# Performance work log

Hardware: AMD Instinct MI355X
Metric: run time of the kernel (lower is better)

## Reference

```python
import math
import jax, jax.numpy as jnp
import numpy as np

B, S, E, H = 2, 2048, 1024, 16
DK = E // H

def setup_inputs() -> dict:
    key = jax.random.key(0)
    ks = jax.random.split(key, 12)
    sc = 1.0 / math.sqrt(E)
    return {
        "x": jax.random.normal(ks[0], (B, S, E), jnp.float32),
        "kv": jax.random.normal(ks[1], (B, S, E), jnp.float32),
        "mask": jax.random.randint(ks[2], (B, S), 0, 2, jnp.int32),
        "attn_bias": jax.random.normal(ks[3], (B, S, S), jnp.float32),
        "WQ_w": jax.random.normal(ks[4], (E, E), jnp.float32) * sc,
        "WQ_b": jnp.zeros((E,), jnp.float32),
        "WK_w": jax.random.normal(ks[5], (E, E), jnp.float32) * sc,
        "WK_b": jnp.zeros((E,), jnp.float32),
        "WV_w": jax.random.normal(ks[6], (E, E), jnp.float32) * sc,
        "WV_b": jnp.zeros((E,), jnp.float32),
        "WO_w": jax.random.normal(ks[7], (E, E), jnp.float32) * sc,
        "WO_b": jnp.zeros((E,), jnp.float32),
    }

def reference(x, kv, mask, attn_bias, WQ_w, WQ_b, WK_w, WK_b, WV_w, WV_b, WO_w, WO_b):
    b, sq, _ = x.shape
    sk = kv.shape[1]
    # projections, split heads: [B,S,E] -> [B,H,S,DK]
    Q = (x @ WQ_w.T + WQ_b).reshape(b, sq, H, DK).transpose(0, 2, 1, 3)
    K = (kv @ WK_w.T + WK_b).reshape(b, sk, H, DK).transpose(0, 2, 1, 3)
    V = (kv @ WV_w.T + WV_b).reshape(b, sk, H, DK).transpose(0, 2, 1, 3)
    # scores [B,H,Sq,Sk]
    T = jnp.einsum('bhqd,bhkd->bhqk', Q, K) / math.sqrt(DK)
    T = T + attn_bias[:, None, :, :]  # 3D bias broadcast over heads
    m2 = jnp.einsum('bi,bj->bij', mask.astype(T.dtype), mask.astype(T.dtype))
    T = jnp.where(m2[:, None, :, :] == 0, jnp.asarray(-1e9, T.dtype), T)
    A = jax.nn.softmax(T, axis=-1)
    out = jnp.einsum('bhqk,bhkd->bhqd', A, V)  # [B,H,Sq,DK]
    out = out.transpose(0, 2, 1, 3).reshape(b, sq, E)
    return out @ WO_w.T + WO_b
```

## Files before the change

kernel.cpp:

```cpp
#include <hip/hip_runtime.h>

#define DEV static __device__ __forceinline__

typedef __attribute__((ext_vector_type(8))) __bf16 bf16x8;
typedef __attribute__((ext_vector_type(4))) float f32x4;

constexpr int CB = 2;
constexpr int CS = 2048;
constexpr int CE = 1024;
constexpr int CH = 16;
constexpr int CD = 64;
constexpr float LOG2E = 1.44269504f;

DEV unsigned short f2bf(float x) {
  unsigned int u = __float_as_uint(x);
  u += 0x7fffu + ((u >> 16) & 1u);
  return (unsigned short)(u >> 16);
}

DEV f32x4 mfma32(bf16x8 a, bf16x8 b, f32x4 c) {
  return __builtin_amdgcn_mfma_f32_16x16x32_bf16(a, b, c, 0, 0, 0);
}

DEV unsigned int cvtpk(float lo, float hi) {
  unsigned int r;
  asm("v_cvt_pk_bf16_f32 %0, %1, %2" : "=v"(r) : "v"(lo), "v"(hi));
  return r;
}

DEV float exp2r(float x) {
#if __has_builtin(__builtin_amdgcn_exp2f)
  return __builtin_amdgcn_exp2f(x);
#else
  float r; asm("v_exp_f32 %0, %1" : "=v"(r) : "v"(x)); return r;
#endif
}

DEV f32x4 unpk(unsigned int a, unsigned int b) {
  f32x4 r;
  r[0] = __uint_as_float(a << 16);
  r[1] = __uint_as_float(a & 0xffff0000u);
  r[2] = __uint_as_float(b << 16);
  r[3] = __uint_as_float(b & 0xffff0000u);
  return r;
}

DEV void stage16(const void* g, void* l) {
  __builtin_amdgcn_global_load_lds(
      (const __attribute__((address_space(1))) unsigned int*)g,
      (__attribute__((address_space(3))) unsigned int*)l, 16, 0, 0);
}

DEV void cvt_body(long i, const float* __restrict__ x, const float* __restrict__ kv,
                  const float* __restrict__ w0, const float* __restrict__ w1,
                  const float* __restrict__ w2, const float* __restrict__ w3,
                  unsigned short* __restrict__ out) {
  const long NE = (long)CB * CS * CE;
  const long WE = (long)CE * CE;
  const float* src;
  long off = i;
  if (i < NE) {
    src = x;
  } else if (i < 2 * NE) {
    src = kv; off = i - NE;
  } else {
    long j = i - 2 * NE;
    int wi = (int)(j >> 20);
    src = wi == 0 ? w0 : wi == 1 ? w1 : wi == 2 ? w2 : w3;
    off = j & (WE - 1);
  }
  float4 a = *reinterpret_cast<const float4*>(src + off);
  float4 b = *reinterpret_cast<const float4*>(src + off + 4);
  uint4 v;
  v.x = (unsigned int)f2bf(a.x) | ((unsigned int)f2bf(a.y) << 16);
  v.y = (unsigned int)f2bf(a.z) | ((unsigned int)f2bf(a.w) << 16);
  v.z = (unsigned int)f2bf(b.x) | ((unsigned int)f2bf(b.y) << 16);
  v.w = (unsigned int)f2bf(b.z) | ((unsigned int)f2bf(b.w) << 16);
  *reinterpret_cast<uint4*>(out + i) = v;
}

DEV void mbias_body(long idx, const float* __restrict__ bias, const int* __restrict__ mask,
                    unsigned short* __restrict__ mb16) {
  const int b = (int)(idx >> 22);
  const int q = (int)((idx >> 11) & (CS - 1));
  const int k0 = (int)(idx & (CS - 1));
  const bool mq = mask[b * CS + q] != 0;
  const int4 mk0 = *reinterpret_cast<const int4*>(mask + b * CS + k0);
  const int4 mk1 = *reinterpret_cast<const int4*>(mask + b * CS + k0 + 4);
  const float4 b0 = *reinterpret_cast<const float4*>(bias + idx);
  const float4 b1 = *reinterpret_cast<const float4*>(bias + idx + 4);
  const float NEG = -1e9f * LOG2E;
  float v[8];
  if (mq) {
    v[0] = (mk0.x != 0) ? b0.x * LOG2E : NEG;
    v[1] = (mk0.y != 0) ? b0.y * LOG2E : NEG;
    v[2] = (mk0.z != 0) ? b0.z * LOG2E : NEG;
    v[3] = (mk0.w != 0) ? b0.w * LOG2E : NEG;
    v[4] = (mk1.x != 0) ? b1.x * LOG2E : NEG;
    v[5] = (mk1.y != 0) ? b1.y * LOG2E : NEG;
    v[6] = (mk1.z != 0) ? b1.z * LOG2E : NEG;
    v[7] = (mk1.w != 0) ? b1.w * LOG2E : NEG;
  } else {
#pragma unroll
    for (int j = 0; j < 8; j++) v[j] = 0.f;
  }
  uint4 o;
  o.x = cvtpk(v[0], v[1]); o.y = cvtpk(v[2], v[3]);
  o.z = cvtpk(v[4], v[5]); o.w = cvtpk(v[6], v[7]);
  *reinterpret_cast<uint4*>(mb16 + idx) = o;
}

__global__ __launch_bounds__(256) void prep_all(const float* __restrict__ x,
                                                const float* __restrict__ kv,
                                                const float* __restrict__ w0,
                                                const float* __restrict__ w1,
                                                const float* __restrict__ w2,
                                                const float* __restrict__ w3,
                                                unsigned short* __restrict__ outcvt,
                                                const float* __restrict__ bias,
                                                const int* __restrict__ mask,
                                                unsigned short* __restrict__ mb16) {
  const long CVTB = (2 * (long)CB * CS * CE + 4 * (long)CE * CE) / 2048;
  if (blockIdx.x < CVTB) {
    cvt_body(((long)blockIdx.x * 256 + threadIdx.x) * 8, x, kv, w0, w1, w2, w3, outcvt);
  } else {
    mbias_body(((long)(blockIdx.x - CVTB) * 256 + threadIdx.x) * 8, bias, mask, mb16);
  }
}

__global__ __launch_bounds__(256) void cvt_all(const float* __restrict__ x,
                                               const float* __restrict__ kv,
                                               const float* __restrict__ w0,
                                               const float* __restrict__ w1,
                                               const float* __restrict__ w2,
                                               const float* __restrict__ w3,
                                               unsigned short* __restrict__ out) {
  cvt_body(((long)blockIdx.x * 256 + threadIdx.x) * 8, x, kv, w0, w1, w2, w3, out);
}
__global__ __launch_bounds__(256) void mk_mbias(const float* __restrict__ bias,
                                                const int* __restrict__ mask,
                                                unsigned short* __restrict__ mb16) {
  mbias_body(((long)blockIdx.x * 256 + threadIdx.x) * 8, bias, mask, mb16);
}

__global__ __launch_bounds__(512) void gemm_qkv(const unsigned short* __restrict__ xb,
                                                const unsigned short* __restrict__ kvb,
                                                const unsigned short* __restrict__ Wall,
                                                const float* __restrict__ bq,
                                                const float* __restrict__ bk,
                                                const float* __restrict__ bv,
                                                unsigned short* __restrict__ Qb) {
  __shared__ __align__(16) unsigned char ldsA[32768];
  __shared__ __align__(16) unsigned char ldsB[32768];
  const long NE = (long)CB * CS * CE;
  const long WE = (long)CE * CE;
  const int which = blockIdx.y >> 2;
  const int n0 = (blockIdx.y & 3) * 256;
  const int m0 = blockIdx.x * 256;
  const unsigned char* Ab = (const unsigned char*)(which == 0 ? xb : kvb);
  const unsigned char* Bb = (const unsigned char*)(Wall + (long)which * WE);
  const float* bias = which == 0 ? bq : which == 1 ? bk : bv;

  const int tid = threadIdx.x;
  const int lane = tid & 63, w = tid >> 6;
  const int wr = w >> 2, wc = w & 3;
  const int g = lane >> 4, rr = lane & 15;

  const int srow = tid >> 2;
  const int scsw = ((tid & 3) * 16) ^ (((tid >> 5) & 1) << 5);
  const unsigned char* apR0 = Ab + ((long)(m0 + srow) * CE) * 2 + scsw;
  const unsigned char* apR1 = Ab + ((long)(m0 + 128 + srow) * CE) * 2 + scsw;
  const unsigned char* bpR0 = Bb + ((long)(n0 + srow) * CE) * 2 + scsw;
  const unsigned char* bpR1 = Bb + ((long)(n0 + 128 + srow) * CE) * 2 + scsw;

  const int cswz = (g * 16) ^ (((rr >> 3) & 1) << 5);
  const unsigned char* rbA = ldsA + wr * 8192 + rr * 64 + cswz;
  const unsigned char* rbB = ldsB + wc * 4096 + rr * 64 + cswz;

  f32x4 acc[8][4] = {};

  auto stA = [&](int buf) {
    stage16(apR0, ldsA + buf * 16384 + w * 1024);
    stage16(apR1, ldsA + buf * 16384 + 8192 + w * 1024);
    apR0 += 64; apR1 += 64;
  };
  auto stB = [&](int buf) {
    stage16(bpR0, ldsB + buf * 16384 + w * 1024);
    stage16(bpR1, ldsB + buf * 16384 + 8192 + w * 1024);
    bpR0 += 64; bpR1 += 64;
  };

  stB(0);
  stA(0);
  stB(1);
  asm volatile("s_waitcnt vmcnt(3)" ::: "memory");
  __builtin_amdgcn_s_barrier();

  auto group = [&](int buf) {
    bf16x8 ar[4], br[4];
#pragma unroll
    for (int ii = 0; ii < 4; ii++)
      ar[ii] = *reinterpret_cast<const bf16x8*>(rbA + buf * 16384 + ii * 1024);
#pragma unroll
    for (int j = 0; j < 4; j++)
      br[j] = *reinterpret_cast<const bf16x8*>(rbB + buf * 16384 + j * 1024);
    stA(buf ^ 1);
    __builtin_amdgcn_s_barrier();
    asm volatile("s_waitcnt lgkmcnt(0)" ::: "memory");
    __builtin_amdgcn_sched_barrier(0);
    __builtin_amdgcn_s_setprio(1);
#pragma unroll
    for (int ii = 0; ii < 4; ii++)
#pragma unroll
      for (int j = 0; j < 4; j++)
        acc[ii][j] = mfma32(ar[ii], br[j], acc[ii][j]);
    __builtin_amdgcn_s_setprio(0);
    asm volatile("s_waitcnt vmcnt(4)" ::: "memory");
    __builtin_amdgcn_s_barrier();
#pragma unroll
    for (int ii = 0; ii < 4; ii++)
      ar[ii] = *reinterpret_cast<const bf16x8*>(rbA + buf * 16384 + 4096 + ii * 1024);
    stB(buf);
    __builtin_amdgcn_s_barrier();
    asm volatile("s_waitcnt lgkmcnt(0)" ::: "memory");
    __builtin_amdgcn_sched_barrier(0);
    __builtin_amdgcn_s_setprio(1);
#pragma unroll
    for (int ii = 0; ii < 4; ii++)
#pragma unroll
      for (int j = 0; j < 4; j++)
        acc[4 + ii][j] = mfma32(ar[ii], br[j], acc[4 + ii][j]);
    __builtin_amdgcn_s_setprio(0);
    asm volatile("s_waitcnt vmcnt(3)" ::: "memory");
    __builtin_amdgcn_s_barrier();
  };

#pragma unroll 1
  for (int it = 0; it < 16; ++it) {
    group(0);
    group(1);
  }
  asm volatile("s_waitcnt vmcnt(0)" ::: "memory");

  const float scale = which == 0 ? 0.125f * LOG2E : 1.0f;
#pragma unroll
  for (int i = 0; i < 8; i++) {
#pragma unroll
    for (int j = 0; j < 4; j++) {
      const int colg = n0 + wc * 64 + j * 16 + rr;
      const float bvv = bias[colg];
      if (which == 2) {
        const int rowbase = m0 + wr * 128 + i * 16 + g * 4;
        const int bb = rowbase >> 11, s = rowbase & 2047;
        const int hh = colg >> 6, d = colg & 63;
        uint2 val;
        val.x = (unsigned int)f2bf(acc[i][j][0] + bvv) | ((unsigned int)f2bf(acc[i][j][1] + bvv) << 16);
        val.y = (unsigned int)f2bf(acc[i][j][2] + bvv) | ((unsigned int)f2bf(acc[i][j][3] + bvv) << 16);
        *reinterpret_cast<uint2*>(Qb + 2 * NE + ((long)((bb * CH + hh) * CD + d)) * CS + s) = val;
      } else {
        unsigned short* outp = Qb + (long)which * NE;
#pragma unroll
        for (int r = 0; r < 4; r++) {
          const int row = m0 + wr * 128 + i * 16 + g * 4 + r;
          outp[(long)row * CE + colg] = f2bf((acc[i][j][r] + bvv) * scale);
        }
      }
    }
  }
}

__global__ __launch_bounds__(256) void gemm_wo(const unsigned short* __restrict__ A,
                                               const unsigned short* __restrict__ W,
                                               const float* __restrict__ bias,
                                               float* __restrict__ out) {
  __shared__ __align__(16) unsigned short As[128 * 64];
  __shared__ __align__(16) unsigned short Bs[64 * 64];
  const int tid = threadIdx.x;
  const int lane = tid & 63, wave = tid >> 6;
  const int wm = (wave >> 1) * 64, wn = (wave & 1) * 32;
  const int g = lane >> 4, rr = lane & 15;
  const int m0 = blockIdx.x * 128, n0 = blockIdx.y * 64;
  const int K = CE;
  f32x4 acc[4][2] = {};

  for (int k0 = 0; k0 < K; k0 += 64) {
#pragma unroll
    for (int t = 0; t < 4; t++) {
      const int u = t * 256 + tid;
      const int row = u >> 3, ce = (u & 7) * 8;
      stage16(A + (long)(m0 + row) * K + k0 + ce, (char*)As + (t * 256 + (tid & 192)) * 16);
    }
#pragma unroll
    for (int t = 0; t < 2; t++) {
      const int u = t * 256 + tid;
      const int row = u >> 3, ce = (u & 7) * 8;
      stage16(W + (long)(n0 + row) * K + k0 + ce, (char*)Bs + (t * 256 + (tid & 192)) * 16);
    }
    __syncthreads();
#pragma unroll
    for (int kk = 0; kk < 2; kk++) {
      bf16x8 af[4], bfr[2];
#pragma unroll
      for (int i = 0; i < 4; i++)
        af[i] = *reinterpret_cast<const bf16x8*>(&As[(wm + i * 16 + rr) * 64 + kk * 32 + g * 8]);
#pragma unroll
      for (int j = 0; j < 2; j++)
        bfr[j] = *reinterpret_cast<const bf16x8*>(&Bs[(wn + j * 16 + rr) * 64 + kk * 32 + g * 8]);
#pragma unroll
      for (int i = 0; i < 4; i++)
#pragma unroll
        for (int j = 0; j < 2; j++)
          acc[i][j] = mfma32(af[i], bfr[j], acc[i][j]);
    }
    __syncthreads();
  }

#pragma unroll
  for (int i = 0; i < 4; i++)
#pragma unroll
    for (int j = 0; j < 2; j++) {
      const int colg = n0 + wn + j * 16 + rr;
      const float bvv = bias[colg];
#pragma unroll
      for (int r = 0; r < 4; r++) {
        const int row = m0 + wm + i * 16 + g * 4 + r;
        out[(long)row * CE + colg] = acc[i][j][r] + bvv;
      }
    }
}

__global__ __launch_bounds__(256, 2) void attn_kernel(const unsigned short* __restrict__ Qb,
                                                      const unsigned short* __restrict__ Kb,
                                                      const unsigned short* __restrict__ Vtw,
                                                      const unsigned short* __restrict__ mb16,
                                                      const int* __restrict__ mask,
                                                      unsigned short* __restrict__ AO) {
  __shared__ __align__(16) unsigned char lds[65536];
  const int h = blockIdx.x, qt = blockIdx.y, b = blockIdx.z;
  const int tid = threadIdx.x;
  const int lane = tid & 63, w = tid >> 6;
  const int g = lane >> 4, c = lane & 15;
  const int qbase = qt * 128 + w * 32;

  bf16x8 qf[2][2];
#pragma unroll
  for (int qb = 0; qb < 2; qb++) {
    const unsigned short* Qrow = Qb + ((long)b * CS + qbase + qb * 16 + c) * CE + h * CD;
    qf[qb][0] = *reinterpret_cast<const bf16x8*>(Qrow + g * 8);
    qf[qb][1] = *reinterpret_cast<const bf16x8*>(Qrow + 32 + g * 8);
    if (mask[b * CS + qbase + qb * 16 + c] == 0) {
      qf[qb][0] = bf16x8{}; qf[qb][1] = bf16x8{};
    }
  }

  const unsigned char *kg[4], *vg[4];
  {
    const unsigned char* Ksrc = (const unsigned char*)(Kb + (long)b * CS * CE + h * CD);
    const unsigned char* Vsrc = (const unsigned char*)(Vtw + (long)(b * CH + h) * CD * CS);
    const int rr8 = lane >> 3;
    const int csw = ((lane & 7) << 4) ^ (rr8 << 4);
#pragma unroll
    for (int t = 0; t < 4; t++) {
      const int krow = t * 32 + w * 8 + rr8;
      const int key = (krow & 96) + ((krow >> 2) & 3) * 8 + ((krow >> 4) & 1) * 4 + (krow & 3);
      kg[t] = Ksrc + (long)key * (CE * 2) + csw;
      const int vrow = (t & 1) * 32 + w * 8 + rr8;
      vg[t] = Vsrc + (long)vrow * (CS * 2) + (t >> 1) * 128 + csw;
    }
  }
  const int sw = (c & 7) << 4;
  const unsigned char* rb0 = lds + c * 128 + ((g * 16) ^ sw);
  const unsigned char* rb1 = lds + c * 128 + ((64 + g * 16) ^ sw);

  const unsigned short* mbp0 = mb16 + ((long)b * CS + qbase + c) * CS + g * 8;
  const unsigned short* mbp1 = mb16 + ((long)b * CS + qbase + 16 + c) * CS + g * 8;

  f32x4 o[2][4] = {};
  f32x4 lsum4[2] = {};
  uint4 mbr[2][4];

  auto stage = [&](int bo) {
    unsigned char* kbuf = lds + bo;
    unsigned char* vbuf = lds + bo + 16384;
#pragma unroll
    for (int t = 0; t < 4; t++) {
      stage16(kg[t], kbuf + t * 4096 + w * 1024);
      stage16(vg[t], vbuf + (t >> 1) * 8192 + (t & 1) * 4096 + w * 1024);
      kg[t] += 128 * CE * 2;
      vg[t] += 128 * 2;
    }
  };
  auto load_mb = [&](bool adv) {
#pragma unroll
    for (int kb = 0; kb < 4; kb++) {
      mbr[0][kb] = *reinterpret_cast<const uint4*>(mbp0 + kb * 32);
      mbr[1][kb] = *reinterpret_cast<const uint4*>(mbp1 + kb * 32);
    }
    if (adv) { mbp0 += 128; mbp1 += 128; }
  };

  auto compute = [&](int bo, bool adv) {
    f32x4 sf[2][8];
    __builtin_amdgcn_s_setprio(1);
#pragma unroll
    for (int cb = 0; cb < 8; cb++) {
      const bf16x8 kf0 = *reinterpret_cast<const bf16x8*>(rb0 + bo + cb * 2048);
      const bf16x8 kf1 = *reinterpret_cast<const bf16x8*>(rb1 + bo + cb * 2048);
#pragma unroll
      for (int qb = 0; qb < 2; qb++) {
        const uint4 m = mbr[qb][cb >> 1];
        const f32x4 ci = (cb & 1) ? unpk(m.z, m.w) : unpk(m.x, m.y);
        f32x4 t = mfma32(kf0, qf[qb][0], ci);
        sf[qb][cb] = mfma32(kf1, qf[qb][1], t);
      }
    }
    __builtin_amdgcn_s_setprio(0);
    load_mb(adv);
    uint4 pw[2][4];
#pragma unroll
    for (int qb = 0; qb < 2; qb++)
#pragma unroll
      for (int kb = 0; kb < 4; kb++)
#pragma unroll
        for (int half = 0; half < 2; half++) {
          const int cb = 2 * kb + half;
          f32x4 pv;
          pv[0] = exp2r(sf[qb][cb][0]);
          pv[1] = exp2r(sf[qb][cb][1]);
          pv[2] = exp2r(sf[qb][cb][2]);
          pv[3] = exp2r(sf[qb][cb][3]);
          lsum4[qb] = lsum4[qb] + pv;
          if (half == 0) { pw[qb][kb].x = cvtpk(pv[0], pv[1]); pw[qb][kb].y = cvtpk(pv[2], pv[3]); }
          else           { pw[qb][kb].z = cvtpk(pv[0], pv[1]); pw[qb][kb].w = cvtpk(pv[2], pv[3]); }
        }
    __builtin_amdgcn_s_setprio(1);
#pragma unroll
    for (int nb = 0; nb < 4; nb++) {
#pragma unroll
      for (int kb = 0; kb < 4; kb++) {
        const unsigned char* rbx = (kb & 1) ? rb1 : rb0;
        const bf16x8 vf = *reinterpret_cast<const bf16x8*>(
            rbx + bo + 16384 + (kb >> 1) * 8192 + nb * 2048);
#pragma unroll
        for (int qb = 0; qb < 2; qb++)
          o[qb][nb] = mfma32(vf, __builtin_bit_cast(bf16x8, pw[qb][kb]), o[qb][nb]);
      }
    }
    __builtin_amdgcn_s_setprio(0);
  };

  stage(0);
  load_mb(true);
  stage(32768);

#pragma unroll 1
  for (int it = 0; it < 8; ++it) {
    asm volatile("s_waitcnt vmcnt(16)" ::: "memory");
    __builtin_amdgcn_s_barrier();
    __builtin_amdgcn_sched_barrier(0);
    compute(0, it < 7);
    __builtin_amdgcn_sched_barrier(0);
    __builtin_amdgcn_s_barrier();
    stage(0);
    asm volatile("s_waitcnt vmcnt(16)" ::: "memory");
    __builtin_amdgcn_s_barrier();
    __builtin_amdgcn_sched_barrier(0);
    compute(32768, it < 7);
    __builtin_amdgcn_sched_barrier(0);
    __builtin_amdgcn_s_barrier();
    stage(32768);
  }

#pragma unroll
  for (int qb = 0; qb < 2; qb++) {
    float lsum = (lsum4[qb][0] + lsum4[qb][1]) + (lsum4[qb][2] + lsum4[qb][3]);
    lsum += __shfl_xor(lsum, 16, 64);
    lsum += __shfl_xor(lsum, 32, 64);
    const float linv = 1.0f / lsum;
    unsigned short* Orow = AO + ((long)b * CS + qbase + qb * 16 + c) * CE + h * CD;
#pragma unroll
    for (int nb = 0; nb < 4; nb++) {
      uint2 val;
      val.x = (unsigned int)f2bf(o[qb][nb][0] * linv) | ((unsigned int)f2bf(o[qb][nb][1] * linv) << 16);
      val.y = (unsigned int)f2bf(o[qb][nb][2] * linv) | ((unsigned int)f2bf(o[qb][nb][3] * linv) << 16);
      *reinterpret_cast<uint2*>(Orow + nb * 16 + g * 4) = val;
    }
  }
  asm volatile("s_waitcnt vmcnt(0)" ::: "memory");
}

extern "C" void kernel_launch(void* const* d_in, const int* in_sizes, int n_in,
                              void* d_out, int out_size, void* d_ws, size_t ws_size,
                              hipStream_t stream) {
  (void)in_sizes; (void)n_in; (void)out_size;
  const float* x    = (const float*)d_in[0];
  const float* kv   = (const float*)d_in[1];
  const int*   mask = (const int*)d_in[2];
  const float* ab   = (const float*)d_in[3];
  const float* WQw  = (const float*)d_in[4];
  const float* WQb  = (const float*)d_in[5];
  const float* WKw  = (const float*)d_in[6];
  const float* WKb  = (const float*)d_in[7];
  const float* WVw  = (const float*)d_in[8];
  const float* WVb  = (const float*)d_in[9];
  const float* WOw  = (const float*)d_in[10];
  const float* WOb  = (const float*)d_in[11];
  float* out = (float*)d_out;

  const long NE = (long)CB * CS * CE;
  const long WE = (long)CE * CE;
  unsigned short* ws  = (unsigned short*)d_ws;
  unsigned short* xb  = ws;
  unsigned short* kvb = xb + NE;
  unsigned short* wqb = kvb + NE;
  unsigned short* wob = wqb + 3 * WE;
  unsigned short* Qb  = wob + WE;
  unsigned short* AO  = Qb + 3 * NE;

  const long TOT = 2 * NE + 4 * WE;
  const long MBE = (long)CB * CS * CS;
  const long needShorts = 8 * NE + 4 * WE;
  const bool fused = ws_size >= (size_t)needShorts * 2;

  if (fused) {
    unsigned short* mb16 = AO + NE;
    prep_all<<<(int)((TOT + MBE) / 2048), 256, 0, stream>>>(x, kv, WQw, WKw, WVw, WOw, xb,
                                                            ab, mask, mb16);
    gemm_qkv<<<dim3(16, 12), 512, 0, stream>>>(xb, kvb, wqb, WQb, WKb, WVb, Qb);
    attn_kernel<<<dim3(CH, CS / 128, CB), 256, 0, stream>>>(
        Qb, Qb + NE, Qb + 2 * NE, mb16, mask, AO);
  } else {
    unsigned short* mb16 = xb;
    cvt_all<<<(int)(TOT / 2048), 256, 0, stream>>>(x, kv, WQw, WKw, WVw, WOw, xb);
    gemm_qkv<<<dim3(16, 12), 512, 0, stream>>>(xb, kvb, wqb, WQb, WKb, WVb, Qb);
    mk_mbias<<<(int)(MBE / 2048), 256, 0, stream>>>(ab, mask, mb16);
    attn_kernel<<<dim3(CH, CS / 128, CB), 256, 0, stream>>>(
        Qb, Qb + NE, Qb + 2 * NE, mb16, mask, AO);
  }

  gemm_wo<<<dim3(32, 16), 256, 0, stream>>>(AO, wob, WOb, out);
}
```

Before: 136.4 us.

## Fuse fp32-to-bf16 activation conversion into QKV GEMM A-tile loads

The QKV projection GEMM now reads fp32 x and kv directly into registers, converts them to bf16 and writes them into LDS. This replaces the separate prep pass that converted the activations to bf16 in global memory, so the bf16 copies of x and kv are no longer written and read back. The B side still uses async global-to-LDS staging, and the prep kernel only converts the weights and builds the mask-bias. The non-fused fallback path is removed and the wait counts are retuned. In exchange the GEMM reads twice as many A bytes, and the A loads now go through registers with explicit LDS writes, which adds VGPR pressure and changes how loads overlap with compute.

```diff
diff --git a/kernel.cpp b/kernel.cpp
--- a/kernel.cpp
+++ b/kernel.cpp
@@ -51,31 +51,18 @@
       (__attribute__((address_space(3))) unsigned int*)l, 16, 0, 0);
 }
 
-DEV void cvt_body(long i, const float* __restrict__ x, const float* __restrict__ kv,
-                  const float* __restrict__ w0, const float* __restrict__ w1,
-                  const float* __restrict__ w2, const float* __restrict__ w3,
-                  unsigned short* __restrict__ out) {
-  const long NE = (long)CB * CS * CE;
+DEV void wcvt_body(long i, const float* __restrict__ w0, const float* __restrict__ w1,
+                   const float* __restrict__ w2, const float* __restrict__ w3,
+                   unsigned short* __restrict__ out) {
   const long WE = (long)CE * CE;
-  const float* src;
-  long off = i;
-  if (i < NE) {
-    src = x;
-  } else if (i < 2 * NE) {
-    src = kv; off = i - NE;
-  } else {
-    long j = i - 2 * NE;
-    int wi = (int)(j >> 20);
-    src = wi == 0 ? w0 : wi == 1 ? w1 : wi == 2 ? w2 : w3;
-    off = j & (WE - 1);
-  }
+  const int wi = (int)(i >> 20);
+  const float* src = wi == 0 ? w0 : wi == 1 ? w1 : wi == 2 ? w2 : w3;
+  const long off = i & (WE - 1);
   float4 a = *reinterpret_cast<const float4*>(src + off);
   float4 b = *reinterpret_cast<const float4*>(src + off + 4);
   uint4 v;
-  v.x = (unsigned int)f2bf(a.x) | ((unsigned int)f2bf(a.y) << 16);
-  v.y = (unsigned int)f2bf(a.z) | ((unsigned int)f2bf(a.w) << 16);
-  v.z = (unsigned int)f2bf(b.x) | ((unsigned int)f2bf(b.y) << 16);
-  v.w = (unsigned int)f2bf(b.z) | ((unsigned int)f2bf(b.w) << 16);
+  v.x = cvtpk(a.x, a.y); v.y = cvtpk(a.z, a.w);
+  v.z = cvtpk(b.x, b.y); v.w = cvtpk(b.z, b.w);
   *reinterpret_cast<uint4*>(out + i) = v;
 }
 
@@ -110,41 +97,24 @@
   *reinterpret_cast<uint4*>(mb16 + idx) = o;
 }
 
-__global__ __launch_bounds__(256) void prep_all(const float* __restrict__ x,
-                                                const float* __restrict__ kv,
-                                                const float* __restrict__ w0,
+__global__ __launch_bounds__(256) void prep_all(const float* __restrict__ w0,
                                                 const float* __restrict__ w1,
                                                 const float* __restrict__ w2,
                                                 const float* __restrict__ w3,
-                                                unsigned short* __restrict__ outcvt,
+                                                unsigned short* __restrict__ wout,
                                                 const float* __restrict__ bias,
                                                 const int* __restrict__ mask,
                                                 unsigned short* __restrict__ mb16) {
-  const long CVTB = (2 * (long)CB * CS * CE + 4 * (long)CE * CE) / 2048;
-  if (blockIdx.x < CVTB) {
-    cvt_body(((long)blockIdx.x * 256 + threadIdx.x) * 8, x, kv, w0, w1, w2, w3, outcvt);
+  const long WCB = (4L * CE * CE) / 2048;
+  if (blockIdx.x < WCB) {
+    wcvt_body(((long)blockIdx.x * 256 + threadIdx.x) * 8, w0, w1, w2, w3, wout);
   } else {
-    mbias_body(((long)(blockIdx.x - CVTB) * 256 + threadIdx.x) * 8, bias, mask, mb16);
-  }
-}
-
-__global__ __launch_bounds__(256) void cvt_all(const float* __restrict__ x,
-                                               const float* __restrict__ kv,
-                                               const float* __restrict__ w0,
-                                               const float* __restrict__ w1,
-                                               const float* __restrict__ w2,
-                                               const float* __restrict__ w3,
-                                               unsigned short* __restrict__ out) {
-  cvt_body(((long)blockIdx.x * 256 + threadIdx.x) * 8, x, kv, w0, w1, w2, w3, out);
-}
-__global__ __launch_bounds__(256) void mk_mbias(const float* __restrict__ bias,
-                                                const int* __restrict__ mask,
-                                                unsigned short* __restrict__ mb16) {
-  mbias_body(((long)blockIdx.x * 256 + threadIdx.x) * 8, bias, mask, mb16);
-}
-
-__global__ __launch_bounds__(512) void gemm_qkv(const unsigned short* __restrict__ xb,
-                                                const unsigned short* __restrict__ kvb,
+    mbias_body(((long)(blockIdx.x - WCB) * 256 + threadIdx.x) * 8, bias, mask, mb16);
+  }
+}
+
+__global__ __launch_bounds__(512) void gemm_qkv(const float* __restrict__ xf,
+                                                const float* __restrict__ kvf,
                                                 const unsigned short* __restrict__ Wall,
                                                 const float* __restrict__ bq,
                                                 const float* __restrict__ bk,
@@ -157,7 +127,7 @@
   const int which = blockIdx.y >> 2;
   const int n0 = (blockIdx.y & 3) * 256;
   const int m0 = blockIdx.x * 256;
-  const unsigned char* Ab = (const unsigned char*)(which == 0 ? xb : kvb);
+  const float* Ax = which == 0 ? xf : kvf;
   const unsigned char* Bb = (const unsigned char*)(Wall + (long)which * WE);
   const float* bias = which == 0 ? bq : which == 1 ? bk : bv;
 
@@ -167,9 +137,12 @@
   const int g = lane >> 4, rr = lane & 15;
 
   const int srow = tid >> 2;
+  const int ecol = ((tid & 3) * 8) ^ (((tid >> 5) & 1) * 16);
+  const float* afp0 = Ax + (long)(m0 + srow) * CE + ecol;
+  const float* afp1 = Ax + (long)(m0 + 128 + srow) * CE + ecol;
+  const float* afb0 = afp0;
+  const float* afb1 = afp1;
   const int scsw = ((tid & 3) * 16) ^ (((tid >> 5) & 1) << 5);
-  const unsigned char* apR0 = Ab + ((long)(m0 + srow) * CE) * 2 + scsw;
-  const unsigned char* apR1 = Ab + ((long)(m0 + 128 + srow) * CE) * 2 + scsw;
   const unsigned char* bpR0 = Bb + ((long)(n0 + srow) * CE) * 2 + scsw;
   const unsigned char* bpR1 = Bb + ((long)(n0 + 128 + srow) * CE) * 2 + scsw;
 
@@ -178,11 +151,25 @@
   const unsigned char* rbB = ldsB + wc * 4096 + rr * 64 + cswz;
 
   f32x4 acc[8][4] = {};
-
-  auto stA = [&](int buf) {
-    stage16(apR0, ldsA + buf * 16384 + w * 1024);
-    stage16(apR1, ldsA + buf * 16384 + 8192 + w * 1024);
-    apR0 += 64; apR1 += 64;
+  float4 afr0, afr1, afr2, afr3;
+
+  auto loadA = [&](bool junk) {
+    const float* p0 = junk ? afb0 : afp0;
+    const float* p1 = junk ? afb1 : afp1;
+    afr0 = *reinterpret_cast<const float4*>(p0);
+    afr1 = *reinterpret_cast<const float4*>(p0 + 4);
+    afr2 = *reinterpret_cast<const float4*>(p1);
+    afr3 = *reinterpret_cast<const float4*>(p1 + 4);
+    if (!junk) { afp0 += 32; afp1 += 32; }
+  };
+  auto writeA = [&](int buf) {
+    uint4 w0v, w1v;
+    w0v.x = cvtpk(afr0.x, afr0.y); w0v.y = cvtpk(afr0.z, afr0.w);
+    w0v.z = cvtpk(afr1.x, afr1.y); w0v.w = cvtpk(afr1.z, afr1.w);
+    w1v.x = cvtpk(afr2.x, afr2.y); w1v.y = cvtpk(afr2.z, afr2.w);
+    w1v.z = cvtpk(afr3.x, afr3.y); w1v.w = cvtpk(afr3.z, afr3.w);
+    *reinterpret_cast<uint4*>(ldsA + buf * 16384 + tid * 16) = w0v;
+    *reinterpret_cast<uint4*>(ldsA + buf * 16384 + 8192 + tid * 16) = w1v;
   };
   auto stB = [&](int buf) {
     stage16(bpR0, ldsB + buf * 16384 + w * 1024);
@@ -190,13 +177,17 @@
     bpR0 += 64; bpR1 += 64;
   };
 
+  loadA(false);
   stB(0);
-  stA(0);
+  asm volatile("s_waitcnt vmcnt(2)" ::: "memory");
+  writeA(0);
+  loadA(false);
   stB(1);
-  asm volatile("s_waitcnt vmcnt(3)" ::: "memory");
+  asm volatile("s_waitcnt vmcnt(6)" ::: "memory");
+  asm volatile("s_waitcnt lgkmcnt(0)" ::: "memory");
   __builtin_amdgcn_s_barrier();
 
-  auto group = [&](int buf) {
+  auto group = [&](int buf, bool junk) {
     bf16x8 ar[4], br[4];
 #pragma unroll
     for (int ii = 0; ii < 4; ii++)
@@ -204,7 +195,8 @@
 #pragma unroll
     for (int j = 0; j < 4; j++)
       br[j] = *reinterpret_cast<const bf16x8*>(rbB + buf * 16384 + j * 1024);
-    stA(buf ^ 1);
+    asm volatile("s_waitcnt vmcnt(2)" ::: "memory");
+    writeA(buf ^ 1);
     __builtin_amdgcn_s_barrier();
     asm volatile("s_waitcnt lgkmcnt(0)" ::: "memory");
     __builtin_amdgcn_sched_barrier(0);
@@ -215,11 +207,11 @@
       for (int j = 0; j < 4; j++)
         acc[ii][j] = mfma32(ar[ii], br[j], acc[ii][j]);
     __builtin_amdgcn_s_setprio(0);
-    asm volatile("s_waitcnt vmcnt(4)" ::: "memory");
     __builtin_amdgcn_s_barrier();
 #pragma unroll
     for (int ii = 0; ii < 4; ii++)
       ar[ii] = *reinterpret_cast<const bf16x8*>(rbA + buf * 16384 + 4096 + ii * 1024);
+    loadA(junk);
     stB(buf);
     __builtin_amdgcn_s_barrier();
     asm volatile("s_waitcnt lgkmcnt(0)" ::: "memory");
@@ -231,14 +223,14 @@
       for (int j = 0; j < 4; j++)
         acc[4 + ii][j] = mfma32(ar[ii], br[j], acc[4 + ii][j]);
     __builtin_amdgcn_s_setprio(0);
-    asm volatile("s_waitcnt vmcnt(3)" ::: "memory");
+    asm volatile("s_waitcnt vmcnt(6)" ::: "memory");
     __builtin_amdgcn_s_barrier();
   };
 
 #pragma unroll 1
   for (int it = 0; it < 16; ++it) {
-    group(0);
-    group(1);
+    group(0, it == 15);
+    group(1, it == 15);
   }
   asm volatile("s_waitcnt vmcnt(0)" ::: "memory");
 
@@ -492,7 +484,7 @@
 extern "C" void kernel_launch(void* const* d_in, const int* in_sizes, int n_in,
                               void* d_out, int out_size, void* d_ws, size_t ws_size,
                               hipStream_t stream) {
-  (void)in_sizes; (void)n_in; (void)out_size;
+  (void)in_sizes; (void)n_in; (void)out_size; (void)ws_size;
   const float* x    = (const float*)d_in[0];
   const float* kv   = (const float*)d_in[1];
   const int*   mask = (const int*)d_in[2];
@@ -510,33 +502,22 @@
   const long NE = (long)CB * CS * CE;
   const long WE = (long)CE * CE;
   unsigned short* ws  = (unsigned short*)d_ws;
-  unsigned short* xb  = ws;
-  unsigned short* kvb = xb + NE;
-  unsigned short* wqb = kvb + NE;
+  unsigned short* wqb = ws;
   unsigned short* wob = wqb + 3 * WE;
   unsigned short* Qb  = wob + WE;
   unsigned short* AO  = Qb + 3 * NE;
-
-  const long TOT = 2 * NE + 4 * WE;
+  unsigned short* mb16 = AO + NE;
+
+  const long WCE = 4 * WE;
   const long MBE = (long)CB * CS * CS;
-  const long needShorts = 8 * NE + 4 * WE;
-  const bool fused = ws_size >= (size_t)needShorts * 2;
-
-  if (fused) {
-    unsigned short* mb16 = AO + NE;
-    prep_all<<<(int)((TOT + MBE) / 2048), 256, 0, stream>>>(x, kv, WQw, WKw, WVw, WOw, xb,
-                                                            ab, mask, mb16);
-    gemm_qkv<<<dim3(16, 12), 512, 0, stream>>>(xb, kvb, wqb, WQb, WKb, WVb, Qb);
-    attn_kernel<<<dim3(CH, CS / 128, CB), 256, 0, stream>>>(
-        Qb, Qb + NE, Qb + 2 * NE, mb16, mask, AO);
-  } else {
-    unsigned short* mb16 = xb;
-    cvt_all<<<(int)(TOT / 2048), 256, 0, stream>>>(x, kv, WQw, WKw, WVw, WOw, xb);
-    gemm_qkv<<<dim3(16, 12), 512, 0, stream>>>(xb, kvb, wqb, WQb, WKb, WVb, Qb);
-    mk_mbias<<<(int)(MBE / 2048), 256, 0, stream>>>(ab, mask, mb16);
-    attn_kernel<<<dim3(CH, CS / 128, CB), 256, 0, stream>>>(
-        Qb, Qb + NE, Qb + 2 * NE, mb16, mask, AO);
-  }
+
+  prep_all<<<(int)((WCE + MBE) / 2048), 256, 0, stream>>>(WQw, WKw, WVw, WOw, wqb,
+                                                          ab, mask, mb16);
+
+  gemm_qkv<<<dim3(16, 12), 512, 0, stream>>>(x, kv, wqb, WQb, WKb, WVb, Qb);
+
+  attn_kernel<<<dim3(CH, CS / 128, CB), 256, 0, stream>>>(
+      Qb, Qb + NE, Qb + 2 * NE, mb16, mask, AO);
 
   gemm_wo<<<dim3(32, 16), 256, 0, stream>>>(AO, wob, WOb, out);
 }
```

Result: no change. 138.2 us (+1.4%).
